# Kernel optimization log

Measured on AMD Instinct MI355X. Metric: run time of the kernel, lower is better.

The kernel has to match this reference:

```python
import jax, jax.numpy as jnp
import numpy as np

NUM_LAYERS = 3
BUFFER_SIZE = 5
RECENCY = 0.9
LOW_POWER_K = 8

B, N, S, C = 8, 8192, 64, 16


def setup_inputs() -> dict:
    key = jax.random.key(0)
    ks = jax.random.split(key, 8)
    return {
        "x": jax.random.normal(ks[0], (B, N, S), jnp.float32),
        "entanglement": jax.random.normal(ks[1], (N, S), jnp.float32),
        # mixing initialized as identity in the module; perturb slightly so it is non-trivial
        "mixing": jnp.eye(N, dtype=jnp.float32) + 0.01 * jax.random.normal(ks[2], (N, N), jnp.float32),
        "readout_w": jax.random.normal(ks[3], (S, S), jnp.float32) / np.sqrt(S).astype(np.float32),
        "enc_w": jax.random.normal(ks[4], (C, S), jnp.float32) / np.sqrt(S).astype(np.float32),
        "enc_b": jnp.zeros((C,), jnp.float32),
        "dec_w": jax.random.normal(ks[5], (S, C), jnp.float32) / np.sqrt(C).astype(np.float32),
        "dec_b": jnp.zeros((S,), jnp.float32),
    }


def _temporal_proximity_scaling(stack, recency_factor):
    # stack: [T, N, S] of buffered activations, stack[-1] most recent.
    # Recency-weighted mean: most recent weight 1, older decayed by recency_factor.
    T = stack.shape[0]
    w = recency_factor ** jnp.arange(T - 1, -1, -1, dtype=stack.dtype)  # [T]
    return jnp.einsum('t,tns->ns', w, stack) / jnp.sum(w)


def _low_power_collapse(s, k):
    # keep top-k |values| per neuron row, zero the rest
    a = jnp.abs(s)
    vals, _ = jax.lax.top_k(a, k)           # [N, k]
    thr = vals[:, -1:]                       # kth largest magnitude per row
    return jnp.where(a >= thr, s, jnp.zeros_like(s))


def reference(x, entanglement, mixing, readout_w, enc_w, enc_b, dec_w, dec_b):
    gate = jax.nn.sigmoid(entanglement)[None]  # [1, N, S]
    buf = []  # ShortTermBuffer contents, vectorized over all neurons: list of [N, S]
    ns = jnp.zeros((N, S), x.dtype)
    for _ in range(NUM_LAYERS):
        # NOTE: the torch code prunes/decays/resets neuron_states at the top of each
        # layer but immediately overwrites it with x.mean(0) -> dead code, omitted.
        x = x * gate
        x = jnp.einsum('bns,nm->bms', x, mixing)
        ns = jnp.mean(x, axis=0)  # [N, S]
        buf.append(ns)
        buf = buf[-BUFFER_SIZE:]
        stack = jnp.stack(buf, axis=0)        # [T, N, S], T = min(layer+1, BUFFER_SIZE)
        ns = _temporal_proximity_scaling(stack, RECENCY)
        # advanced_state_collapse via autoencoder (importance_threshold=0.0 -> always reconstruct)
        h = jax.nn.relu(ns @ enc_w.T + enc_b)  # [N, C]
        ns = h @ dec_w.T + dec_b               # [N, S]
        ns = _low_power_collapse(ns, LOW_POWER_K)
    out = x @ readout_w.T  # Linear(S, S, bias=False)
    # torch forward returns only readout(x); neuron_states is a mutated buffer.
    # We also return it so the memory-bound per-neuron state pipeline is not DCE'd.
    return out, ns
```

## Files before the change

### kernel.cpp

```cpp
#include <hip/hip_runtime.h>

#define NN 8192
#define SS 64
#define BSD 512
#define NS (NN*SS)
#define NBS (NN*BSD)

typedef __attribute__((ext_vector_type(4))) _Float16 f16x4;
typedef __attribute__((ext_vector_type(8))) _Float16 f16x8;
typedef __attribute__((ext_vector_type(4))) float f32x4;

#define GLOAD_LDS16(gptr, lptr) \
    __builtin_amdgcn_global_load_lds((const __attribute__((address_space(1))) void*)(gptr), \
                                     (__attribute__((address_space(3))) void*)(lptr), 16, 0, 0)

__device__ __forceinline__ int kmap(int lane, int e) {
    return ((lane >> 4) << 2) + (e & 3) + ((e >> 2) << 4);
}

__global__ void sigmoid_gate_kernel(const float* __restrict__ ent, float* __restrict__ gate) {
    int i = blockIdx.x * 256 + threadIdx.x;
    gate[i] = 1.0f / (1.0f + expf(-ent[i]));
}

__device__ __forceinline__ void pack_tile(const _Float16 (*Lh)[136], const _Float16 (*Ll)[136],
                                          char* tile, int t) {
    #pragma unroll
    for (int j = 0; j < 4; ++j) {
        int idx  = j * 256 + t;
        int blk  = idx >> 7;
        int kk   = (idx >> 6) & 1;
        int lane = idx & 63;
        int col  = blk * 16 + (lane & 15);
        int kb   = kk * 32;
        f16x8 hv, lv;
        #pragma unroll
        for (int e = 0; e < 8; ++e) {
            int k = kb + kmap(lane, e);
            hv[e] = Lh[k][col];
            lv[e] = Ll[k][col];
        }
        *(f16x8*)(tile + idx * 16)         = hv;
        *(f16x8*)(tile + 16384 + idx * 16) = lv;
    }
}

__global__ __launch_bounds__(256) void convA_kernel(const float* __restrict__ Mx,
                                                    char* __restrict__ Ab) {
    __shared__ _Float16 Lh[64][136];
    __shared__ _Float16 Ll[64][136];
    const int t = threadIdx.x;
    const int kt = blockIdx.x, mt = blockIdx.y;
    const int k0 = kt * 64, m0 = mt * 128;
    #pragma unroll
    for (int i = 0; i < 8; ++i) {
        int e = i * 256 + t;
        int kr = e >> 5, m4 = (e & 31) << 2;
        float4 v = *(const float4*)&Mx[(size_t)(k0 + kr) * NN + m0 + m4];
        int d = (k0 + kr) - (m0 + m4);
        if (d == 0) v.x -= 1.0f;
        if (d == 1) v.y -= 1.0f;
        if (d == 2) v.z -= 1.0f;
        if (d == 3) v.w -= 1.0f;
        f16x4 h, l;
        h[0] = (_Float16)v.x; l[0] = (_Float16)(v.x - (float)h[0]);
        h[1] = (_Float16)v.y; l[1] = (_Float16)(v.y - (float)h[1]);
        h[2] = (_Float16)v.z; l[2] = (_Float16)(v.z - (float)h[2]);
        h[3] = (_Float16)v.w; l[3] = (_Float16)(v.w - (float)h[3]);
        *(f16x4*)&Lh[kr][m4] = h;
        *(f16x4*)&Ll[kr][m4] = l;
    }
    __syncthreads();
    pack_tile(Lh, Ll, Ab + ((size_t)(mt * 128 + kt) << 15), t);
}

__device__ __forceinline__ void pack_B(const _Float16 (*Lh)[520],
                                       const _Float16 (*Nh)[72], const _Float16 (*Nl)[72],
                                       char* Bb, char* Nb, int kt, int t) {
    #pragma unroll
    for (int j = 0; j < 16; ++j) {
        int idx = j * 256 + t;
        int nbt = idx >> 10, w = idx & 1023;
        int blk = w >> 7, kk = (w >> 6) & 1, lane = w & 63;
        int col = nbt * 128 + blk * 16 + (lane & 15);
        int kb = kk * 32;
        f16x8 hv;
        #pragma unroll
        for (int e = 0; e < 8; ++e)
            hv[e] = Lh[kb + kmap(lane, e)][col];
        *(f16x8*)(Bb + (((size_t)kt * 4 + nbt) << 14) + w * 16) = hv;
    }
    #pragma unroll
    for (int j = 0; j < 4; ++j) {
        int idx = j * 256 + t;
        int nbt = idx >> 8, r = idx & 255;
        int part = r >> 7, kk = (r >> 6) & 1, lane = r & 63;
        int s = nbt * 16 + (lane & 15);
        int kb = kk * 32;
        f16x8 v;
        #pragma unroll
        for (int e = 0; e < 8; ++e) {
            int k = kb + kmap(lane, e);
            v[e] = part ? Nl[k][s] : Nh[k][s];
        }
        *(f16x8*)(Nb + (((size_t)kt * 4 + nbt) << 12) + part * 2048 + kk * 1024 + lane * 16) = v;
    }
}

__global__ __launch_bounds__(256) void prep0_kernel(const float* __restrict__ x,
                                                    const float* __restrict__ gate,
                                                    float* __restrict__ X,
                                                    char* __restrict__ Bb,
                                                    char* __restrict__ Nb,
                                                    float* __restrict__ mg32) {
    __shared__ _Float16 Lh[64][520];
    __shared__ _Float16 Nh[64][72];
    __shared__ _Float16 Nl[64][72];
    const int t = threadIdx.x;
    const int kt = blockIdx.x;
    const int n0 = kt * 64;
    #pragma unroll
    for (int i = 0; i < 4; ++i) {
        int e = i * 256 + t;
        int kr = e >> 4;
        int s4 = (e & 15) << 2;
        float4 g = *(const float4*)&gate[(size_t)(n0 + kr) * 64 + s4];
        float4 ms = make_float4(0.f, 0.f, 0.f, 0.f);
        #pragma unroll
        for (int b = 0; b < 8; ++b) {
            float4 v = *(const float4*)&x[((size_t)b * NN + n0 + kr) * 64 + s4];
            ms.x += v.x; ms.y += v.y; ms.z += v.z; ms.w += v.w;
            v.x *= g.x; v.y *= g.y; v.z *= g.z; v.w *= g.w;
            *(float4*)&X[(size_t)(n0 + kr) * BSD + b * 64 + s4] = v;
            f16x4 h;
            h[0] = (_Float16)v.x; h[1] = (_Float16)v.y;
            h[2] = (_Float16)v.z; h[3] = (_Float16)v.w;
            *(f16x4*)&Lh[kr][b * 64 + s4] = h;
        }
        float4 mg4;
        mg4.x = ms.x * 0.125f * g.x; mg4.y = ms.y * 0.125f * g.y;
        mg4.z = ms.z * 0.125f * g.z; mg4.w = ms.w * 0.125f * g.w;
        *(float4*)&mg32[(size_t)(n0 + kr) * 64 + s4] = mg4;
        f16x4 mh, ml;
        mh[0] = (_Float16)mg4.x; ml[0] = (_Float16)(mg4.x - (float)mh[0]);
        mh[1] = (_Float16)mg4.y; ml[1] = (_Float16)(mg4.y - (float)mh[1]);
        mh[2] = (_Float16)mg4.z; ml[2] = (_Float16)(mg4.z - (float)mh[2]);
        mh[3] = (_Float16)mg4.w; ml[3] = (_Float16)(mg4.w - (float)mh[3]);
        *(f16x4*)&Nh[kr][s4] = mh;
        *(f16x4*)&Nl[kr][s4] = ml;
    }
    __syncthreads();
    pack_B(Lh, Nh, Nl, Bb, Nb, kt, t);
}

__global__ __launch_bounds__(256) void gateconv_kernel(float* __restrict__ X,
                                                       const float* __restrict__ gate,
                                                       const float* __restrict__ nsprev,
                                                       char* __restrict__ Bb,
                                                       char* __restrict__ Nb,
                                                       float* __restrict__ mg32) {
    __shared__ _Float16 Lh[64][520];
    __shared__ _Float16 Nh[64][72];
    __shared__ _Float16 Nl[64][72];
    const int t = threadIdx.x;
    const int kt = blockIdx.x;
    const int n0 = kt * 64;
    #pragma unroll
    for (int i = 0; i < 32; ++i) {
        int e = i * 256 + t;
        int kr = e >> 7;
        int c4 = (e & 127) << 2;
        float4 v = *(const float4*)&X[(size_t)(n0 + kr) * BSD + c4];
        float4 g = *(const float4*)&gate[(size_t)(n0 + kr) * 64 + (c4 & 63)];
        v.x *= g.x; v.y *= g.y; v.z *= g.z; v.w *= g.w;
        *(float4*)&X[(size_t)(n0 + kr) * BSD + c4] = v;
        f16x4 h;
        h[0] = (_Float16)v.x; h[1] = (_Float16)v.y;
        h[2] = (_Float16)v.z; h[3] = (_Float16)v.w;
        *(f16x4*)&Lh[kr][c4] = h;
    }
    #pragma unroll
    for (int i = 0; i < 4; ++i) {
        int e = i * 256 + t;
        int kr = e >> 4;
        int s4 = (e & 15) << 2;
        float4 p = *(const float4*)&nsprev[(size_t)(n0 + kr) * 64 + s4];
        float4 g = *(const float4*)&gate[(size_t)(n0 + kr) * 64 + s4];
        float4 mg4;
        mg4.x = p.x * g.x; mg4.y = p.y * g.y; mg4.z = p.z * g.z; mg4.w = p.w * g.w;
        *(float4*)&mg32[(size_t)(n0 + kr) * 64 + s4] = mg4;
        f16x4 mh, ml;
        mh[0] = (_Float16)mg4.x; ml[0] = (_Float16)(mg4.x - (float)mh[0]);
        mh[1] = (_Float16)mg4.y; ml[1] = (_Float16)(mg4.y - (float)mh[1]);
        mh[2] = (_Float16)mg4.z; ml[2] = (_Float16)(mg4.z - (float)mh[2]);
        mh[3] = (_Float16)mg4.w; ml[3] = (_Float16)(mg4.w - (float)mh[3]);
        *(f16x4*)&Nh[kr][s4] = mh;
        *(f16x4*)&Nl[kr][s4] = ml;
    }
    __syncthreads();
    pack_B(Lh, Nh, Nl, Bb, Nb, kt, t);
}

__global__ __launch_bounds__(512) void gemm_f16_kernel(const char* __restrict__ Ab,
                                                       const char* __restrict__ Bb,
                                                       const char* __restrict__ Nb,
                                                       float* X,
                                                       const float* __restrict__ mg,
                                                       float* __restrict__ nsout) {
    __shared__ char lds[2][53248];
    const int t = threadIdx.x;
    const int L = blockIdx.x;
    const int mt  = (L & 7) + ((L >> 5) << 3);
    const int nbt = (L >> 3) & 3;
    const int lane = t & 63, wid = t >> 6;
    const int wr = wid >> 2, wc = wid & 3;
    const int fins = wid & 3;

    auto stage = [&](int buf, int kt) {
        const char* ga = Ab + (((size_t)mt * 128 + kt) << 15);
        const char* gb = Bb + (((size_t)kt * 4 + nbt) << 14);
        const char* gn = Nb + (((size_t)kt * 4 + nbt) << 12);
        char* la = lds[buf];
        GLOAD_LDS16(ga + wid * 2048 + lane * 16,                 la + wid * 2048);
        GLOAD_LDS16(ga + wid * 2048 + 1024 + lane * 16,          la + wid * 2048 + 1024);
        GLOAD_LDS16(ga + 16384 + wid * 2048 + lane * 16,         la + 16384 + wid * 2048);
        GLOAD_LDS16(ga + 16384 + wid * 2048 + 1024 + lane * 16,  la + 16384 + wid * 2048 + 1024);
        GLOAD_LDS16(gb + wid * 2048 + lane * 16,                 la + 32768 + wid * 2048);
        GLOAD_LDS16(gb + wid * 2048 + 1024 + lane * 16,          la + 32768 + wid * 2048 + 1024);
        if (wid < 4)
            GLOAD_LDS16(gn + wid * 1024 + lane * 16,             la + 49152 + wid * 1024);
    };

    f32x4 accm[4][2];
    #pragma unroll
    for (int fi = 0; fi < 4; ++fi) {
        accm[fi][0] = (f32x4){0.f, 0.f, 0.f, 0.f};
        accm[fi][1] = (f32x4){0.f, 0.f, 0.f, 0.f};
    }
    f32x4 accn = (f32x4){0.f, 0.f, 0.f, 0.f};

    stage(0, 0);
    for (int kt = 0; kt < 128; ++kt) {
        const int cur = kt & 1;
        if (kt < 127) {
            stage(cur ^ 1, kt + 1);
            if (wid < 4) asm volatile("s_waitcnt vmcnt(7)" ::: "memory");
            else         asm volatile("s_waitcnt vmcnt(6)" ::: "memory");
        } else {
            asm volatile("s_waitcnt vmcnt(0)" ::: "memory");
        }
        __builtin_amdgcn_s_barrier();
        __builtin_amdgcn_sched_barrier(0);
        const char* base = lds[cur];
        const char* A_ = base + wr * 8192 + lane * 16;
        const char* Bm = base + 32768 + wc * 4096 + lane * 16;
        const char* Bn = base + 49152 + lane * 16;
        #pragma unroll
        for (int kk = 0; kk < 2; ++kk) {
            const int ko = kk * 1024;
            f16x8 bm0 = *(const f16x8*)(Bm + ko);
            f16x8 bm1 = *(const f16x8*)(Bm + 2048 + ko);
            f16x8 bnh = *(const f16x8*)(Bn + ko);
            f16x8 bnl = *(const f16x8*)(Bn + 2048 + ko);
            f16x8 ahn = *(const f16x8*)(A_ + fins * 2048 + ko);
            f16x8 aln = *(const f16x8*)(A_ + 16384 + fins * 2048 + ko);
            #pragma unroll
            for (int fi = 0; fi < 4; ++fi) {
                f16x8 ah = *(const f16x8*)(A_ + fi * 2048 + ko);
                accm[fi][0] = __builtin_amdgcn_mfma_f32_16x16x32_f16(ah, bm0, accm[fi][0], 0, 0, 0);
                accm[fi][1] = __builtin_amdgcn_mfma_f32_16x16x32_f16(ah, bm1, accm[fi][1], 0, 0, 0);
            }
            accn = __builtin_amdgcn_mfma_f32_16x16x32_f16(ahn, bnh, accn, 0, 0, 0);
            accn = __builtin_amdgcn_mfma_f32_16x16x32_f16(ahn, bnl, accn, 0, 0, 0);
            accn = __builtin_amdgcn_mfma_f32_16x16x32_f16(aln, bnh, accn, 0, 0, 0);
        }
        __builtin_amdgcn_sched_barrier(0);
        __builtin_amdgcn_s_barrier();
    }

    const int row0 = mt * 128 + wr * 64 + ((lane >> 4) << 2);
    const int col0 = nbt * 128 + wc * 32 + (lane & 15);
    #pragma unroll
    for (int fi = 0; fi < 4; ++fi)
        #pragma unroll
        for (int fj = 0; fj < 2; ++fj)
            #pragma unroll
            for (int j = 0; j < 4; ++j) {
                size_t idx = (size_t)(row0 + fi * 16 + j) * BSD + col0 + fj * 16;
                X[idx] = accm[fi][fj][j] + X[idx];
            }
    const int nr0 = mt * 128 + wid * 16 + ((lane >> 4) << 2);
    const int nc  = nbt * 16 + (lane & 15);
    #pragma unroll
    for (int j = 0; j < 4; ++j) {
        size_t nidx = (size_t)(nr0 + j) * 64 + nc;
        nsout[nidx] = accn[j] + mg[nidx];
    }
}

__global__ __launch_bounds__(256) void readout_kernel(const float* __restrict__ X3,
                                                      const float* __restrict__ W,
                                                      float* __restrict__ out) {
    __shared__ float Wt[64][65];
    __shared__ float xr[512];
    const int n = blockIdx.x;
    const int t = threadIdx.x;
    for (int e = t; e < 4096; e += 256) {
        int s = e >> 6, sp = e & 63;
        Wt[sp][s] = W[e];
    }
    xr[t]       = X3[(size_t)n * BSD + t];
    xr[t + 256] = X3[(size_t)n * BSD + 256 + t];
    __syncthreads();
    const int b1 = t >> 6;
    const int s  = t & 63;
    float acc0 = 0.0f, acc1 = 0.0f;
    #pragma unroll
    for (int sp = 0; sp < 64; ++sp) {
        float w = Wt[sp][s];
        acc0 += w * xr[b1 * 64 + sp];
        acc1 += w * xr[(b1 + 4) * 64 + sp];
    }
    out[((size_t)b1 * NN + n) * SS + s]       = acc0;
    out[((size_t)(b1 + 4) * NN + n) * SS + s] = acc1;
}

__global__ void nsfinal_kernel(const float* __restrict__ ns0,
                               const float* __restrict__ enc_w, const float* __restrict__ enc_b,
                               const float* __restrict__ dec_w, const float* __restrict__ dec_b,
                               float* __restrict__ out_ns) {
    int gtid = blockIdx.x * 256 + threadIdx.x;
    int lane = gtid & 63;
    const float r = 0.9f;
    const float wsum = 1.0f + r + r * r;
    float tns = (ns0[gtid] * (r * r) + ns0[NS + gtid] * r + ns0[2 * NS + gtid]) / wsum;
    float v = dec_b[lane];
    #pragma unroll
    for (int c = 0; c < 16; ++c) {
        float p = tns * enc_w[c * 64 + lane];
        #pragma unroll
        for (int off = 32; off; off >>= 1) p += __shfl_xor(p, off, 64);
        float h = fmaxf(p + enc_b[c], 0.0f);
        v += h * dec_w[lane * 16 + c];
    }
    float av = fabsf(v);
    int cnt = 0;
    for (int j = 0; j < 64; ++j) {
        float o = __shfl(av, j, 64);
        cnt += (o > av) ? 1 : 0;
    }
    out_ns[gtid] = (cnt < 8) ? v : 0.0f;
}

extern "C" void kernel_launch(void* const* d_in, const int* in_sizes, int n_in,
                              void* d_out, int out_size, void* d_ws, size_t ws_size,
                              hipStream_t stream) {
    const float* x      = (const float*)d_in[0];
    const float* ent    = (const float*)d_in[1];
    const float* mixing = (const float*)d_in[2];
    const float* r_w    = (const float*)d_in[3];
    const float* enc_w  = (const float*)d_in[4];
    const float* enc_b  = (const float*)d_in[5];
    const float* dec_w  = (const float*)d_in[6];
    const float* dec_b  = (const float*)d_in[7];
    float* out = (float*)d_out;

    char*  Ab   = (char*)d_ws;
    char*  Bb   = Ab + 268435456ull;
    char*  Nb   = Bb + 8388608ull;
    float* X    = (float*)(Nb + 2097152ull);
    float* mg32 = X + NBS;
    float* ns0  = mg32 + NS;
    float* gate = ns0 + 3 * (size_t)NS;

    sigmoid_gate_kernel<<<NS / 256, 256, 0, stream>>>(ent, gate);
    convA_kernel<<<dim3(128, 64), 256, 0, stream>>>(mixing, Ab);
    prep0_kernel<<<128, 256, 0, stream>>>(x, gate, X, Bb, Nb, mg32);

    for (int l = 0; l < 3; ++l) {
        gemm_f16_kernel<<<256, 512, 0, stream>>>(Ab, Bb, Nb, X, mg32, ns0 + (size_t)l * NS);
        if (l < 2)
            gateconv_kernel<<<128, 256, 0, stream>>>(X, gate, ns0 + (size_t)l * NS, Bb, Nb, mg32);
    }

    readout_kernel<<<NN, 256, 0, stream>>>(X, r_w, out);
    nsfinal_kernel<<<2048, 256, 0, stream>>>(ns0, enc_w, enc_b, dec_w, dec_b, out + NBS);
}
```

Measured before the change: 669.4 us.

## Halve GEMM M-tile to 64 rows with 256-thread blocks and 512-block grid

```diff
diff --git a/kernel.cpp b/kernel.cpp
--- a/kernel.cpp
+++ b/kernel.cpp
@@ -21,28 +21,6 @@
 __global__ void sigmoid_gate_kernel(const float* __restrict__ ent, float* __restrict__ gate) {
     int i = blockIdx.x * 256 + threadIdx.x;
     gate[i] = 1.0f / (1.0f + expf(-ent[i]));
-}
-
-__device__ __forceinline__ void pack_tile(const _Float16 (*Lh)[136], const _Float16 (*Ll)[136],
-                                          char* tile, int t) {
-    #pragma unroll
-    for (int j = 0; j < 4; ++j) {
-        int idx  = j * 256 + t;
-        int blk  = idx >> 7;
-        int kk   = (idx >> 6) & 1;
-        int lane = idx & 63;
-        int col  = blk * 16 + (lane & 15);
-        int kb   = kk * 32;
-        f16x8 hv, lv;
-        #pragma unroll
-        for (int e = 0; e < 8; ++e) {
-            int k = kb + kmap(lane, e);
-            hv[e] = Lh[k][col];
-            lv[e] = Ll[k][col];
-        }
-        *(f16x8*)(tile + idx * 16)         = hv;
-        *(f16x8*)(tile + 16384 + idx * 16) = lv;
-    }
 }
 
 __global__ __launch_bounds__(256) void convA_kernel(const float* __restrict__ Mx,
@@ -71,7 +49,27 @@
         *(f16x4*)&Ll[kr][m4] = l;
     }
     __syncthreads();
-    pack_tile(Lh, Ll, Ab + ((size_t)(mt * 128 + kt) << 15), t);
+    #pragma unroll
+    for (int j = 0; j < 4; ++j) {
+        int idx  = j * 256 + t;
+        int h    = idx >> 9;
+        int w    = idx & 511;
+        int blk  = w >> 7;
+        int kk   = (w >> 6) & 1;
+        int lane = w & 63;
+        int col  = h * 64 + blk * 16 + (lane & 15);
+        int kb   = kk * 32;
+        f16x8 hv, lv;
+        #pragma unroll
+        for (int e = 0; e < 8; ++e) {
+            int k = kb + kmap(lane, e);
+            hv[e] = Lh[k][col];
+            lv[e] = Ll[k][col];
+        }
+        char* tile = Ab + (((size_t)(mt * 2 + h) * 128 + kt) << 14);
+        *(f16x8*)(tile + w * 16)        = hv;
+        *(f16x8*)(tile + 8192 + w * 16) = lv;
+    }
 }
 
 __device__ __forceinline__ void pack_B(const _Float16 (*Lh)[520],
@@ -201,34 +199,33 @@
     pack_B(Lh, Nh, Nl, Bb, Nb, kt, t);
 }
 
-__global__ __launch_bounds__(512) void gemm_f16_kernel(const char* __restrict__ Ab,
+__global__ __launch_bounds__(256) void gemm_f16_kernel(const char* __restrict__ Ab,
                                                        const char* __restrict__ Bb,
                                                        const char* __restrict__ Nb,
                                                        float* X,
                                                        const float* __restrict__ mg,
                                                        float* __restrict__ nsout) {
-    __shared__ char lds[2][53248];
+    __shared__ char lds[2][36864];
     const int t = threadIdx.x;
     const int L = blockIdx.x;
     const int mt  = (L & 7) + ((L >> 5) << 3);
     const int nbt = (L >> 3) & 3;
     const int lane = t & 63, wid = t >> 6;
-    const int wr = wid >> 2, wc = wid & 3;
-    const int fins = wid & 3;
 
     auto stage = [&](int buf, int kt) {
-        const char* ga = Ab + (((size_t)mt * 128 + kt) << 15);
+        const char* ga = Ab + (((size_t)mt * 128 + kt) << 14);
         const char* gb = Bb + (((size_t)kt * 4 + nbt) << 14);
         const char* gn = Nb + (((size_t)kt * 4 + nbt) << 12);
         char* la = lds[buf];
-        GLOAD_LDS16(ga + wid * 2048 + lane * 16,                 la + wid * 2048);
-        GLOAD_LDS16(ga + wid * 2048 + 1024 + lane * 16,          la + wid * 2048 + 1024);
-        GLOAD_LDS16(ga + 16384 + wid * 2048 + lane * 16,         la + 16384 + wid * 2048);
-        GLOAD_LDS16(ga + 16384 + wid * 2048 + 1024 + lane * 16,  la + 16384 + wid * 2048 + 1024);
-        GLOAD_LDS16(gb + wid * 2048 + lane * 16,                 la + 32768 + wid * 2048);
-        GLOAD_LDS16(gb + wid * 2048 + 1024 + lane * 16,          la + 32768 + wid * 2048 + 1024);
-        if (wid < 4)
-            GLOAD_LDS16(gn + wid * 1024 + lane * 16,             la + 49152 + wid * 1024);
+        GLOAD_LDS16(ga + wid * 2048 + lane * 16,               la + wid * 2048);
+        GLOAD_LDS16(ga + wid * 2048 + 1024 + lane * 16,        la + wid * 2048 + 1024);
+        GLOAD_LDS16(ga + 8192 + wid * 2048 + lane * 16,        la + 8192 + wid * 2048);
+        GLOAD_LDS16(ga + 8192 + wid * 2048 + 1024 + lane * 16, la + 8192 + wid * 2048 + 1024);
+        #pragma unroll
+        for (int i = 0; i < 4; ++i)
+            GLOAD_LDS16(gb + wid * 4096 + i * 1024 + lane * 16,
+                        la + 16384 + wid * 4096 + i * 1024);
+        GLOAD_LDS16(gn + wid * 1024 + lane * 16,               la + 32768 + wid * 1024);
     };
 
     f32x4 accm[4][2];
@@ -240,21 +237,15 @@
     f32x4 accn = (f32x4){0.f, 0.f, 0.f, 0.f};
 
     stage(0, 0);
+    asm volatile("s_waitcnt vmcnt(0)" ::: "memory");
+    __builtin_amdgcn_s_barrier();
     for (int kt = 0; kt < 128; ++kt) {
         const int cur = kt & 1;
-        if (kt < 127) {
-            stage(cur ^ 1, kt + 1);
-            if (wid < 4) asm volatile("s_waitcnt vmcnt(7)" ::: "memory");
-            else         asm volatile("s_waitcnt vmcnt(6)" ::: "memory");
-        } else {
-            asm volatile("s_waitcnt vmcnt(0)" ::: "memory");
-        }
-        __builtin_amdgcn_s_barrier();
-        __builtin_amdgcn_sched_barrier(0);
+        if (kt < 127) stage(cur ^ 1, kt + 1);
         const char* base = lds[cur];
-        const char* A_ = base + wr * 8192 + lane * 16;
-        const char* Bm = base + 32768 + wc * 4096 + lane * 16;
-        const char* Bn = base + 49152 + lane * 16;
+        const char* A_ = base + lane * 16;
+        const char* Bm = base + 16384 + wid * 4096 + lane * 16;
+        const char* Bn = base + 32768 + lane * 16;
         #pragma unroll
         for (int kk = 0; kk < 2; ++kk) {
             const int ko = kk * 1024;
@@ -262,8 +253,8 @@
             f16x8 bm1 = *(const f16x8*)(Bm + 2048 + ko);
             f16x8 bnh = *(const f16x8*)(Bn + ko);
             f16x8 bnl = *(const f16x8*)(Bn + 2048 + ko);
-            f16x8 ahn = *(const f16x8*)(A_ + fins * 2048 + ko);
-            f16x8 aln = *(const f16x8*)(A_ + 16384 + fins * 2048 + ko);
+            f16x8 ahn = *(const f16x8*)(A_ + wid * 2048 + ko);
+            f16x8 aln = *(const f16x8*)(A_ + 8192 + wid * 2048 + ko);
             #pragma unroll
             for (int fi = 0; fi < 4; ++fi) {
                 f16x8 ah = *(const f16x8*)(A_ + fi * 2048 + ko);
@@ -274,12 +265,12 @@
             accn = __builtin_amdgcn_mfma_f32_16x16x32_f16(ahn, bnl, accn, 0, 0, 0);
             accn = __builtin_amdgcn_mfma_f32_16x16x32_f16(aln, bnh, accn, 0, 0, 0);
         }
-        __builtin_amdgcn_sched_barrier(0);
+        asm volatile("s_waitcnt vmcnt(0)" ::: "memory");
         __builtin_amdgcn_s_barrier();
     }
 
-    const int row0 = mt * 128 + wr * 64 + ((lane >> 4) << 2);
-    const int col0 = nbt * 128 + wc * 32 + (lane & 15);
+    const int row0 = mt * 64 + ((lane >> 4) << 2);
+    const int col0 = nbt * 128 + wid * 32 + (lane & 15);
     #pragma unroll
     for (int fi = 0; fi < 4; ++fi)
         #pragma unroll
@@ -289,7 +280,7 @@
                 size_t idx = (size_t)(row0 + fi * 16 + j) * BSD + col0 + fj * 16;
                 X[idx] = accm[fi][fj][j] + X[idx];
             }
-    const int nr0 = mt * 128 + wid * 16 + ((lane >> 4) << 2);
+    const int nr0 = mt * 64 + wid * 16 + ((lane >> 4) << 2);
     const int nc  = nbt * 16 + (lane & 15);
     #pragma unroll
     for (int j = 0; j < 4; ++j) {
@@ -378,7 +369,7 @@
     prep0_kernel<<<128, 256, 0, stream>>>(x, gate, X, Bb, Nb, mg32);
 
     for (int l = 0; l < 3; ++l) {
-        gemm_f16_kernel<<<256, 512, 0, stream>>>(Ab, Bb, Nb, X, mg32, ns0 + (size_t)l * NS);
+        gemm_f16_kernel<<<512, 256, 0, stream>>>(Ab, Bb, Nb, X, mg32, ns0 + (size_t)l * NS);
         if (l < 2)
             gateconv_kernel<<<128, 256, 0, stream>>>(X, gate, ns0 + (size_t)l * NS, Bb, Nb, mg32);
     }
```

Result: slower. 683.0 us (+2.0%).
